# Optimization experiments

Measured on AMD Instinct MI355X. Metric: run time of the kernel, lower is better.

Reference implementation:

```python
import jax, jax.numpy as jnp
import numpy as np

B, H, L, N_HEADS = 8192, 1024, 1024, 5

def setup_inputs() -> dict:
    key = jax.random.key(0)
    k1, k2, k3, k4, k5 = jax.random.split(key, 5)
    hidden_state = jax.random.normal(k1, (B, H), dtype=jnp.float32)
    W = jax.random.normal(k2, (N_HEADS, L, H), dtype=jnp.float32) * 0.02  # stacked head weights
    b = jax.random.normal(k3, (N_HEADS, L), dtype=jnp.float32) * 0.02     # stacked head biases
    group = jax.random.randint(k4, (B,), 0, 6, dtype=jnp.int32)
    labels = jax.random.randint(k5, (B,), 0, L, dtype=jnp.int32)
    return {"hidden_state": hidden_state, "W": W, "b": b, "group": group, "labels": labels}

def reference(hidden_state, W, b, group, labels):
    # 5 linear heads in one batched GEMM: [5, B, L]
    all_logits = jnp.einsum("bh,klh->kbl", hidden_state, W) + b[:, None, :]
    # per-row selection by group index (return_logit=True path)
    idx = jnp.clip(group, 0, N_HEADS - 1)
    sel = all_logits[idx, jnp.arange(B)]  # [B, L]
    # group == 5: row filled with broadcast label value (as in original)
    logits = jnp.where((group == 5)[:, None], labels[:, None].astype(jnp.float32), sel)
    return logits
```

## Files before the change

### kernel.cpp

```cpp
#include <hip/hip_runtime.h>
#include <stdint.h>

#define B_ROWS 8192
#define H_DIM 1024
#define L_DIM 1024
#define NH 5

typedef short bf16x8 __attribute__((ext_vector_type(8)));
typedef float f32x4 __attribute__((ext_vector_type(4)));

typedef const __attribute__((address_space(1))) unsigned int* gas_uint_ptr;
typedef __attribute__((address_space(3))) unsigned int* las_uint_ptr;

__device__ __forceinline__ unsigned short f2bf(float f) {
  union { float f; unsigned int u; } v; v.f = f;
  return (unsigned short)((v.u + 0x7FFFu + ((v.u >> 16) & 1u)) >> 16);
}

__device__ __forceinline__ void load_lds16(const void* gsrc, void* ldst) {
  __builtin_amdgcn_global_load_lds((gas_uint_ptr)(uintptr_t)gsrc,
                                   (las_uint_ptr)(uintptr_t)ldst, 16, 0, 0);
}

__global__ void k_conv(const float* __restrict__ hidden, const float* __restrict__ W,
                       const int* __restrict__ group, const int* __restrict__ labels,
                       int* __restrict__ cnt, int* __restrict__ rowlist,
                       unsigned short* __restrict__ Hb, unsigned short* __restrict__ Wb,
                       float* __restrict__ out) {
  const int blk = blockIdx.x;
  const int t = threadIdx.x;
  if (blk < 512) {
    const float4* src = (const float4*)W;
    ushort4* dst = (ushort4*)Wb;
#pragma unroll
    for (int i = 0; i < 10; i++) {
      int idx = (i * 512 + blk) * 256 + t;
      float4 w = src[idx];
      ushort4 o;
      o.x = f2bf(w.x); o.y = f2bf(w.y); o.z = f2bf(w.z); o.w = f2bf(w.w);
      dst[idx] = o;
    }
  } else if (blk < 1536) {
    const int rb = (blk - 512) * 8;
    int gs[8];
#pragma unroll
    for (int r = 0; r < 8; r++) gs[r] = group[rb + r];
#pragma unroll
    for (int r = 0; r < 8; r++) {
      int row = rb + r;
      if (gs[r] == NH) {
        float v = (float)labels[row];
        ((float4*)(out + (size_t)row * L_DIM))[t] = make_float4(v, v, v, v);
      } else {
        float4 h = ((const float4*)(hidden + (size_t)row * H_DIM))[t];
        ushort4 o;
        o.x = f2bf(h.x); o.y = f2bf(h.y); o.z = f2bf(h.z); o.w = f2bf(h.w);
        ((ushort4*)(Hb + (size_t)row * H_DIM))[t] = o;
      }
    }
  } else {
    __shared__ int lcnt[NH];
    __shared__ int lbase[NH];
    if (t < NH) lcnt[t] = 0;
    __syncthreads();
    int b = (blk - 1536) * 256 + t;
    int g = group[b];
    int lpos = -1;
    if (g < NH) lpos = atomicAdd(&lcnt[g], 1);
    __syncthreads();
    if (t < NH) lbase[t] = atomicAdd(&cnt[t], lcnt[t]);
    __syncthreads();
    if (g < NH) rowlist[g * B_ROWS + lbase[g] + lpos] = b;
  }
}

__global__ __launch_bounds__(256, 2)
void k_gemm(const unsigned short* __restrict__ Hb, const unsigned short* __restrict__ Wb,
            const float* __restrict__ bias, const int* __restrict__ cnt,
            const int* __restrict__ rowlist, float* __restrict__ out) {
  const int head = blockIdx.z;
  const int cntg = cnt[head];
  const int rowbase = blockIdx.y * 128;
  if (rowbase >= cntg) return;
  const int n0 = blockIdx.x * 128;

  __shared__ __align__(16) unsigned short As[2][128 * 64];
  __shared__ __align__(16) unsigned short Bs[2][128 * 64];

  const int t = threadIdx.x;
  const int wave = t >> 6, lane = t & 63;
  const int quad = lane >> 4, c16 = lane & 15;
  const int wm = (wave & 1) * 64, wn = (wave >> 1) * 64;

  const unsigned short* Wg = Wb + (size_t)head * L_DIM * H_DIM;
  const int* rl = rowlist + head * B_ROWS;

  const unsigned short* srcA[4];
  const unsigned short* srcB[4];
  int ldso[4];
#pragma unroll
  for (int p = 0; p < 4; p++) {
    int c = p * 256 + t;
    int row = c >> 3;
    int ks = ((c & 7) ^ (row & 7)) * 8;
    int idx = rowbase + row;
    idx = idx < cntg ? idx : cntg - 1;
    srcA[p] = Hb + (size_t)rl[idx] * H_DIM + ks;
    srcB[p] = Wg + (size_t)(n0 + row) * H_DIM + ks;
    ldso[p] = c * 8;
  }

  f32x4 acc[4][4] = {};

#pragma unroll
  for (int p = 0; p < 4; p++) {
    load_lds16(srcA[p], &As[0][ldso[p]]);
    load_lds16(srcB[p], &Bs[0][ldso[p]]);
  }
  __syncthreads();

  for (int kt = 0; kt < H_DIM; kt += 64) {
    const int cur = (kt >> 6) & 1;
    if (kt + 64 < H_DIM) {
      const int nxt = cur ^ 1;
#pragma unroll
      for (int p = 0; p < 4; p++) {
        load_lds16(srcA[p] + kt + 64, &As[nxt][ldso[p]]);
        load_lds16(srcB[p] + kt + 64, &Bs[nxt][ldso[p]]);
      }
    }
#pragma unroll
    for (int kk = 0; kk < 64; kk += 32) {
      bf16x8 af[4], bf[4];
      const int sw = c16 & 7;
      const int colb = (kk >> 4) << 1;
      const int cl = (colb + quad) ^ sw;
#pragma unroll
      for (int i = 0; i < 4; i++) {
        int row = wm + i * 16 + c16;
        af[i] = *(const bf16x8*)(&As[cur][row * 64 + cl * 8]);
      }
#pragma unroll
      for (int j = 0; j < 4; j++) {
        int row = wn + j * 16 + c16;
        bf[j] = *(const bf16x8*)(&Bs[cur][row * 64 + cl * 8]);
      }
#pragma unroll
      for (int i = 0; i < 4; i++)
#pragma unroll
        for (int j = 0; j < 4; j++)
          acc[i][j] = __builtin_amdgcn_mfma_f32_16x16x32_bf16(af[i], bf[j], acc[i][j], 0, 0, 0);
    }
    __syncthreads();
  }

#pragma unroll
  for (int i = 0; i < 4; i++) {
    int rloc0 = wm + i * 16 + quad * 4;
#pragma unroll
    for (int r = 0; r < 4; r++) {
      int idx = rloc0 + r;
      if (rowbase + idx < cntg) {
        int orow = rl[rowbase + idx];
        float* orowp = out + (size_t)orow * L_DIM + n0;
#pragma unroll
        for (int j = 0; j < 4; j++) {
          int n = wn + j * 16 + c16;
          orowp[n] = acc[i][j][r] + bias[head * L_DIM + n0 + n];
        }
      }
    }
  }
}

extern "C" void kernel_launch(void* const* d_in, const int* in_sizes, int n_in,
                              void* d_out, int out_size, void* d_ws, size_t ws_size,
                              hipStream_t stream) {
  const float* hidden = (const float*)d_in[0];
  const float* W      = (const float*)d_in[1];
  const float* bias   = (const float*)d_in[2];
  const int* group    = (const int*)d_in[3];
  const int* labels   = (const int*)d_in[4];
  float* out = (float*)d_out;

  char* ws = (char*)d_ws;
  int* cnt = (int*)ws;
  int* rowlist = (int*)(ws + 256);
  unsigned short* Wb = (unsigned short*)(ws + (1 << 18));
  unsigned short* Hb = (unsigned short*)(ws + (1 << 18) + (size_t)NH * L_DIM * H_DIM * 2);

  hipMemsetAsync(cnt, 0, 64, stream);
  k_conv<<<1568, 256, 0, stream>>>(hidden, W, group, labels, cnt, rowlist, Hb, Wb, out);
  k_gemm<<<dim3(L_DIM / 128, B_ROWS / 128, NH), 256, 0, stream>>>(Hb, Wb, bias, cnt, rowlist, out);
}
```

Baseline: 127.9 us.

## Widen GEMM tile to 128x256 and use nontemporal loads/stores

The GEMM block tile grows from 128x128 to 128x256 output columns, with each wave computing 64x128 and holding 32 accumulators. This raises arithmetic intensity per LDS load and halves the number of blocks, at the cost of more registers and LDS (occupancy bound dropped to 1 block). The change also hoists the bias loads out of the store loop. It uses nontemporal loads and stores for the streaming fp32 input reads and the output writes, to reduce cache pollution.

Result: slower. 148.9 us (+16.4%).

```diff
diff --git a/kernel.cpp b/kernel.cpp
--- a/kernel.cpp
+++ b/kernel.cpp
@@ -30,12 +30,12 @@
   const int blk = blockIdx.x;
   const int t = threadIdx.x;
   if (blk < 512) {
-    const float4* src = (const float4*)W;
+    const f32x4* src = (const f32x4*)W;
     ushort4* dst = (ushort4*)Wb;
 #pragma unroll
     for (int i = 0; i < 10; i++) {
       int idx = (i * 512 + blk) * 256 + t;
-      float4 w = src[idx];
+      f32x4 w = __builtin_nontemporal_load(&src[idx]);
       ushort4 o;
       o.x = f2bf(w.x); o.y = f2bf(w.y); o.z = f2bf(w.z); o.w = f2bf(w.w);
       dst[idx] = o;
@@ -50,9 +50,10 @@
       int row = rb + r;
       if (gs[r] == NH) {
         float v = (float)labels[row];
-        ((float4*)(out + (size_t)row * L_DIM))[t] = make_float4(v, v, v, v);
+        f32x4 fv; fv.x = v; fv.y = v; fv.z = v; fv.w = v;
+        __builtin_nontemporal_store(fv, &((f32x4*)(out + (size_t)row * L_DIM))[t]);
       } else {
-        float4 h = ((const float4*)(hidden + (size_t)row * H_DIM))[t];
+        f32x4 h = __builtin_nontemporal_load(&((const f32x4*)(hidden + (size_t)row * H_DIM))[t]);
         ushort4 o;
         o.x = f2bf(h.x); o.y = f2bf(h.y); o.z = f2bf(h.z); o.w = f2bf(h.w);
         ((ushort4*)(Hb + (size_t)row * H_DIM))[t] = o;
@@ -74,7 +75,7 @@
   }
 }
 
-__global__ __launch_bounds__(256, 2)
+__global__ __launch_bounds__(256, 1)
 void k_gemm(const unsigned short* __restrict__ Hb, const unsigned short* __restrict__ Wb,
             const float* __restrict__ bias, const int* __restrict__ cnt,
             const int* __restrict__ rowlist, float* __restrict__ out) {
@@ -82,22 +83,21 @@
   const int cntg = cnt[head];
   const int rowbase = blockIdx.y * 128;
   if (rowbase >= cntg) return;
-  const int n0 = blockIdx.x * 128;
+  const int n0 = blockIdx.x * 256;
 
   __shared__ __align__(16) unsigned short As[2][128 * 64];
-  __shared__ __align__(16) unsigned short Bs[2][128 * 64];
+  __shared__ __align__(16) unsigned short Bs[2][256 * 64];
 
   const int t = threadIdx.x;
   const int wave = t >> 6, lane = t & 63;
   const int quad = lane >> 4, c16 = lane & 15;
-  const int wm = (wave & 1) * 64, wn = (wave >> 1) * 64;
+  const int wm = (wave & 1) * 64, wn = (wave >> 1) * 128;
 
   const unsigned short* Wg = Wb + (size_t)head * L_DIM * H_DIM;
   const int* rl = rowlist + head * B_ROWS;
 
   const unsigned short* srcA[4];
-  const unsigned short* srcB[4];
-  int ldso[4];
+  int ldsoA[4];
 #pragma unroll
   for (int p = 0; p < 4; p++) {
     int c = p * 256 + t;
@@ -106,17 +106,25 @@
     int idx = rowbase + row;
     idx = idx < cntg ? idx : cntg - 1;
     srcA[p] = Hb + (size_t)rl[idx] * H_DIM + ks;
+    ldsoA[p] = c * 8;
+  }
+  const unsigned short* srcB[8];
+  int ldsoB[8];
+#pragma unroll
+  for (int p = 0; p < 8; p++) {
+    int c = p * 256 + t;
+    int row = c >> 3;
+    int ks = ((c & 7) ^ (row & 7)) * 8;
     srcB[p] = Wg + (size_t)(n0 + row) * H_DIM + ks;
-    ldso[p] = c * 8;
-  }
-
-  f32x4 acc[4][4] = {};
-
-#pragma unroll
-  for (int p = 0; p < 4; p++) {
-    load_lds16(srcA[p], &As[0][ldso[p]]);
-    load_lds16(srcB[p], &Bs[0][ldso[p]]);
-  }
+    ldsoB[p] = c * 8;
+  }
+
+  f32x4 acc[4][8] = {};
+
+#pragma unroll
+  for (int p = 0; p < 4; p++) load_lds16(srcA[p], &As[0][ldsoA[p]]);
+#pragma unroll
+  for (int p = 0; p < 8; p++) load_lds16(srcB[p], &Bs[0][ldsoB[p]]);
   __syncthreads();
 
   for (int kt = 0; kt < H_DIM; kt += 64) {
@@ -124,14 +132,13 @@
     if (kt + 64 < H_DIM) {
       const int nxt = cur ^ 1;
 #pragma unroll
-      for (int p = 0; p < 4; p++) {
-        load_lds16(srcA[p] + kt + 64, &As[nxt][ldso[p]]);
-        load_lds16(srcB[p] + kt + 64, &Bs[nxt][ldso[p]]);
-      }
+      for (int p = 0; p < 4; p++) load_lds16(srcA[p] + kt + 64, &As[nxt][ldsoA[p]]);
+#pragma unroll
+      for (int p = 0; p < 8; p++) load_lds16(srcB[p] + kt + 64, &Bs[nxt][ldsoB[p]]);
     }
 #pragma unroll
     for (int kk = 0; kk < 64; kk += 32) {
-      bf16x8 af[4], bf[4];
+      bf16x8 af[4], bf[8];
       const int sw = c16 & 7;
       const int colb = (kk >> 4) << 1;
       const int cl = (colb + quad) ^ sw;
@@ -141,19 +148,22 @@
         af[i] = *(const bf16x8*)(&As[cur][row * 64 + cl * 8]);
       }
 #pragma unroll
-      for (int j = 0; j < 4; j++) {
+      for (int j = 0; j < 8; j++) {
         int row = wn + j * 16 + c16;
         bf[j] = *(const bf16x8*)(&Bs[cur][row * 64 + cl * 8]);
       }
 #pragma unroll
       for (int i = 0; i < 4; i++)
 #pragma unroll
-        for (int j = 0; j < 4; j++)
+        for (int j = 0; j < 8; j++)
           acc[i][j] = __builtin_amdgcn_mfma_f32_16x16x32_bf16(af[i], bf[j], acc[i][j], 0, 0, 0);
     }
     __syncthreads();
   }
 
+  float bv[8];
+#pragma unroll
+  for (int j = 0; j < 8; j++) bv[j] = bias[head * L_DIM + n0 + wn + j * 16 + c16];
 #pragma unroll
   for (int i = 0; i < 4; i++) {
     int rloc0 = wm + i * 16 + quad * 4;
@@ -162,11 +172,10 @@
       int idx = rloc0 + r;
       if (rowbase + idx < cntg) {
         int orow = rl[rowbase + idx];
-        float* orowp = out + (size_t)orow * L_DIM + n0;
-#pragma unroll
-        for (int j = 0; j < 4; j++) {
-          int n = wn + j * 16 + c16;
-          orowp[n] = acc[i][j][r] + bias[head * L_DIM + n0 + n];
+        float* orowp = out + (size_t)orow * L_DIM + n0 + wn;
+#pragma unroll
+        for (int j = 0; j < 8; j++) {
+          __builtin_nontemporal_store(acc[i][j][r] + bv[j], &orowp[j * 16 + c16]);
         }
       }
     }
@@ -191,5 +200,5 @@
 
   hipMemsetAsync(cnt, 0, 64, stream);
   k_conv<<<1568, 256, 0, stream>>>(hidden, W, group, labels, cnt, rowlist, Hb, Wb, out);
-  k_gemm<<<dim3(L_DIM / 128, B_ROWS / 128, NH), 256, 0, stream>>>(Hb, Wb, bias, cnt, rowlist, out);
-}
+  k_gemm<<<dim3(L_DIM / 256, B_ROWS / 128, NH), 256, 0, stream>>>(Hb, Wb, bias, cnt, rowlist, out);
+}
```

## Load A fragments directly to registers, drop A LDS tile, add nontemporal accesses

Applied to the files above, without the earlier changes.

The GEMM kernel stops staging the gathered hidden-state tile in LDS. Each lane now loads its A fragments straight from global memory into registers, with a two-set register ping-pong (aP/aQ) across K steps, while only W goes through LDS. This halves LDS use and removes the A LDS reads and writes, at the cost of more VGPRs and less coalesced, redundant global loads, since each A row is read by both N-waves. The conversion and epilogue also switch to nontemporal loads and stores, and the bias values are hoisted out of the row loop.

Measured after the change: 152.5 us. 19.2% more time.

```diff
diff --git a/kernel.cpp b/kernel.cpp
--- a/kernel.cpp
+++ b/kernel.cpp
@@ -30,12 +30,12 @@
   const int blk = blockIdx.x;
   const int t = threadIdx.x;
   if (blk < 512) {
-    const float4* src = (const float4*)W;
+    const f32x4* src = (const f32x4*)W;
     ushort4* dst = (ushort4*)Wb;
 #pragma unroll
     for (int i = 0; i < 10; i++) {
       int idx = (i * 512 + blk) * 256 + t;
-      float4 w = src[idx];
+      f32x4 w = __builtin_nontemporal_load(&src[idx]);
       ushort4 o;
       o.x = f2bf(w.x); o.y = f2bf(w.y); o.z = f2bf(w.z); o.w = f2bf(w.w);
       dst[idx] = o;
@@ -50,9 +50,10 @@
       int row = rb + r;
       if (gs[r] == NH) {
         float v = (float)labels[row];
-        ((float4*)(out + (size_t)row * L_DIM))[t] = make_float4(v, v, v, v);
+        f32x4 fv; fv.x = v; fv.y = v; fv.z = v; fv.w = v;
+        __builtin_nontemporal_store(fv, &((f32x4*)(out + (size_t)row * L_DIM))[t]);
       } else {
-        float4 h = ((const float4*)(hidden + (size_t)row * H_DIM))[t];
+        f32x4 h = __builtin_nontemporal_load(&((const f32x4*)(hidden + (size_t)row * H_DIM))[t]);
         ushort4 o;
         o.x = f2bf(h.x); o.y = f2bf(h.y); o.z = f2bf(h.z); o.w = f2bf(h.w);
         ((ushort4*)(Hb + (size_t)row * H_DIM))[t] = o;
@@ -84,7 +85,6 @@
   if (rowbase >= cntg) return;
   const int n0 = blockIdx.x * 128;
 
-  __shared__ __align__(16) unsigned short As[2][128 * 64];
   __shared__ __align__(16) unsigned short Bs[2][128 * 64];
 
   const int t = threadIdx.x;
@@ -95,65 +95,88 @@
   const unsigned short* Wg = Wb + (size_t)head * L_DIM * H_DIM;
   const int* rl = rowlist + head * B_ROWS;
 
-  const unsigned short* srcA[4];
   const unsigned short* srcB[4];
-  int ldso[4];
+  int ldsoB[4];
 #pragma unroll
   for (int p = 0; p < 4; p++) {
     int c = p * 256 + t;
     int row = c >> 3;
     int ks = ((c & 7) ^ (row & 7)) * 8;
-    int idx = rowbase + row;
+    srcB[p] = Wg + (size_t)(n0 + row) * H_DIM + ks;
+    ldsoB[p] = c * 8;
+  }
+
+  const unsigned short* pA[4];
+#pragma unroll
+  for (int i = 0; i < 4; i++) {
+    int idx = rowbase + wm + i * 16 + c16;
     idx = idx < cntg ? idx : cntg - 1;
-    srcA[p] = Hb + (size_t)rl[idx] * H_DIM + ks;
-    srcB[p] = Wg + (size_t)(n0 + row) * H_DIM + ks;
-    ldso[p] = c * 8;
+    pA[i] = Hb + (size_t)rl[idx] * H_DIM + quad * 8;
   }
 
   f32x4 acc[4][4] = {};
-
-#pragma unroll
-  for (int p = 0; p < 4; p++) {
-    load_lds16(srcA[p], &As[0][ldso[p]]);
-    load_lds16(srcB[p], &Bs[0][ldso[p]]);
-  }
-  __syncthreads();
-
-  for (int kt = 0; kt < H_DIM; kt += 64) {
-    const int cur = (kt >> 6) & 1;
-    if (kt + 64 < H_DIM) {
-      const int nxt = cur ^ 1;
-#pragma unroll
-      for (int p = 0; p < 4; p++) {
-        load_lds16(srcA[p] + kt + 64, &As[nxt][ldso[p]]);
-        load_lds16(srcB[p] + kt + 64, &Bs[nxt][ldso[p]]);
-      }
-    }
+  bf16x8 aP[8], aQ[8];
+
+  auto loada = [&](bf16x8* dst, int kt) {
+#pragma unroll
+    for (int h = 0; h < 2; h++)
+#pragma unroll
+      for (int i = 0; i < 4; i++)
+        dst[h * 4 + i] = *(const bf16x8*)(pA[i] + kt + h * 32);
+  };
+
+  auto compute = [&](const bf16x8* a, int cur) {
 #pragma unroll
     for (int kk = 0; kk < 64; kk += 32) {
-      bf16x8 af[4], bf[4];
+      bf16x8 bfr[4];
       const int sw = c16 & 7;
       const int colb = (kk >> 4) << 1;
       const int cl = (colb + quad) ^ sw;
 #pragma unroll
-      for (int i = 0; i < 4; i++) {
-        int row = wm + i * 16 + c16;
-        af[i] = *(const bf16x8*)(&As[cur][row * 64 + cl * 8]);
-      }
-#pragma unroll
       for (int j = 0; j < 4; j++) {
         int row = wn + j * 16 + c16;
-        bf[j] = *(const bf16x8*)(&Bs[cur][row * 64 + cl * 8]);
+        bfr[j] = *(const bf16x8*)(&Bs[cur][row * 64 + cl * 8]);
       }
 #pragma unroll
       for (int i = 0; i < 4; i++)
 #pragma unroll
         for (int j = 0; j < 4; j++)
-          acc[i][j] = __builtin_amdgcn_mfma_f32_16x16x32_bf16(af[i], bf[j], acc[i][j], 0, 0, 0);
-    }
-    __syncthreads();
-  }
-
+          acc[i][j] = __builtin_amdgcn_mfma_f32_16x16x32_bf16(a[(kk >> 5) * 4 + i], bfr[j],
+                                                              acc[i][j], 0, 0, 0);
+    }
+  };
+
+#pragma unroll
+  for (int p = 0; p < 4; p++) load_lds16(srcB[p], &Bs[0][ldsoB[p]]);
+  loada(aP, 0);
+  __syncthreads();
+
+  for (int kt2 = 0; kt2 < H_DIM; kt2 += 128) {
+    {
+      const int kt = kt2, cur = (kt >> 6) & 1, nxt = cur ^ 1;
+      if (kt + 64 < H_DIM) {
+#pragma unroll
+        for (int p = 0; p < 4; p++) load_lds16(srcB[p] + kt + 64, &Bs[nxt][ldsoB[p]]);
+        loada(aQ, kt + 64);
+      }
+      compute(aP, cur);
+      __syncthreads();
+    }
+    {
+      const int kt = kt2 + 64, cur = (kt >> 6) & 1, nxt = cur ^ 1;
+      if (kt + 64 < H_DIM) {
+#pragma unroll
+        for (int p = 0; p < 4; p++) load_lds16(srcB[p] + kt + 64, &Bs[nxt][ldsoB[p]]);
+        loada(aP, kt + 64);
+      }
+      compute(aQ, cur);
+      __syncthreads();
+    }
+  }
+
+  float bv[4];
+#pragma unroll
+  for (int j = 0; j < 4; j++) bv[j] = bias[head * L_DIM + n0 + wn + j * 16 + c16];
 #pragma unroll
   for (int i = 0; i < 4; i++) {
     int rloc0 = wm + i * 16 + quad * 4;
@@ -162,12 +185,10 @@
       int idx = rloc0 + r;
       if (rowbase + idx < cntg) {
         int orow = rl[rowbase + idx];
-        float* orowp = out + (size_t)orow * L_DIM + n0;
-#pragma unroll
-        for (int j = 0; j < 4; j++) {
-          int n = wn + j * 16 + c16;
-          orowp[n] = acc[i][j][r] + bias[head * L_DIM + n0 + n];
-        }
+        float* orowp = out + (size_t)orow * L_DIM + n0 + wn;
+#pragma unroll
+        for (int j = 0; j < 4; j++)
+          __builtin_nontemporal_store(acc[i][j][r] + bv[j], &orowp[j * 16 + c16]);
       }
     }
   }
@@ -189,7 +210,7 @@
   unsigned short* Wb = (unsigned short*)(ws + (1 << 18));
   unsigned short* Hb = (unsigned short*)(ws + (1 << 18) + (size_t)NH * L_DIM * H_DIM * 2);
 
-  hipMemsetAsync(cnt, 0, 64, stream);
+  (void)hipMemsetAsync(cnt, 0, 64, stream);
   k_conv<<<1568, 256, 0, stream>>>(hidden, W, group, labels, cnt, rowlist, Hb, Wb, out);
   k_gemm<<<dim3(L_DIM / 128, B_ROWS / 128, NH), 256, 0, stream>>>(Hb, Wb, bias, cnt, rowlist, out);
 }
```
